# Performance work log

Measured on AMD Instinct MI355X. Metric: run time of the kernel, lower is better.

The kernel has to match this reference:

```python
import jax, jax.numpy as jnp
import numpy as np

B, IN, U = 16, 1024, 1024


def _wSw(W, S):
    # W: [i,u], S: [b,i,i] -> W^T S W : [b,u,u]
    return jnp.einsum('iu,bij,jv->buv', W, S, W)


def _xSx(x, Wsig):
    # (sum_i x_i^2) * W_Sigma, broadcast over batch
    return jnp.sum(x * x, axis=1)[:, None, None] * Wsig


def _trS(S, Wsig):
    return jnp.trace(S, axis1=1, axis2=2)[:, None, None] * Wsig


def _hadamard_sigma(s1, s2, m1, m2):
    # s1*s2 + diag(m1) s2 diag(m1) + diag(m2) s1 diag(m2)
    return (s1 * s2
            + m1[:, :, None] * s2 * m1[:, None, :]
            + m2[:, :, None] * s1 * m2[:, None, :])


def _act_sigma(g, S):
    # S * outer(g, g)
    return S * (g[:, :, None] * g[:, None, :])


def setup_inputs() -> dict:
    key = jax.random.key(0)
    ks = jax.random.split(key, 16)
    f32 = jnp.float32
    init_mu, ini_sigma = 0.05, -4.6
    inp = {
        'mu_inputs': jax.random.normal(ks[0], (B, IN), f32),
        'sigma_inputs': 0.01 * jax.random.normal(ks[1], (B, IN, IN), f32),
        'prev_state': 0.1 * jax.random.normal(ks[2], (B, U), f32),
        'Sigma_state': 0.01 * jax.random.normal(ks[3], (B, U, U), f32),
        'U_z': init_mu * jax.random.normal(ks[4], (IN, U), f32),
        'uz_sigma': jnp.full((U,), ini_sigma, f32),
        'W_z': init_mu * jax.random.normal(ks[5], (U, U), f32),
        'wz_sigma': jnp.full((U,), ini_sigma, f32),
        'U_r': init_mu * jax.random.normal(ks[6], (IN, U), f32),
        'ur_sigma': jnp.full((U,), ini_sigma, f32),
        'W_r': init_mu * jax.random.normal(ks[7], (U, U), f32),
        'wr_sigma': jnp.full((U,), ini_sigma, f32),
        'U_h': init_mu * jax.random.normal(ks[8], (IN, U), f32),
        'uh_sigma': jnp.full((U,), ini_sigma, f32),
        'W_h': init_mu * jax.random.normal(ks[9], (U, U), f32),
        'wh_sigma': jnp.full((U,), ini_sigma, f32),
    }
    return inp


def reference(mu_inputs, sigma_inputs, prev_state, Sigma_state,
              U_z, uz_sigma, W_z, wz_sigma,
              U_r, ur_sigma, W_r, wr_sigma,
              U_h, uh_sigma, W_h, wh_sigma):
    sp = jax.nn.softplus
    # ---- z gate ----
    pre_z = mu_inputs @ U_z + prev_state @ W_z
    z = jax.nn.sigmoid(pre_z)
    Uz_S, Wz_S = jnp.diag(sp(uz_sigma)), jnp.diag(sp(wz_sigma))
    Sigma_zz = (_wSw(U_z, sigma_inputs) + _xSx(mu_inputs, Uz_S) + _trS(sigma_inputs, Uz_S)
                + _wSw(W_z, Sigma_state) + _xSx(prev_state, Wz_S) + _trS(Sigma_state, Wz_S))
    Sigma_z = _act_sigma(z * (1.0 - z), Sigma_zz)  # analytic d sigmoid
    # ---- r gate ----
    pre_r = mu_inputs @ U_r + prev_state @ W_r
    r = jax.nn.sigmoid(pre_r)
    Ur_S, Wr_S = jnp.diag(sp(ur_sigma)), jnp.diag(sp(wr_sigma))
    Sigma_rr = (_wSw(U_r, sigma_inputs) + _xSx(mu_inputs, Ur_S) + _trS(sigma_inputs, Ur_S)
                + _wSw(W_r, Sigma_state) + _xSx(prev_state, Wr_S) + _trS(Sigma_state, Wr_S))
    Sigma_r = _act_sigma(r * (1.0 - r), Sigma_rr)
    # ---- h gate ----
    sr = prev_state * r
    pre_h = mu_inputs @ U_h + sr @ W_h
    h = jnp.tanh(pre_h)
    Uh_S, Wh_S = jnp.diag(sp(uh_sigma)), jnp.diag(sp(wh_sigma))
    sigma_g = _hadamard_sigma(Sigma_state, Sigma_r, prev_state, r)
    Sigma_hh = (_wSw(U_h, sigma_inputs) + _xSx(mu_inputs, Uh_S) + _trS(sigma_inputs, Uh_S)
                + _wSw(W_h, sigma_g) + _xSx(sr, Wh_S) + _trS(sigma_g, Wh_S))
    Sigma_h = _act_sigma(1.0 - h * h, Sigma_hh)  # analytic d tanh
    # ---- combine ----
    mu_out = z * prev_state + (1.0 - z) * h
    sigma_a = _hadamard_sigma(Sigma_z, Sigma_state, z, prev_state)
    sigma_b = _hadamard_sigma(Sigma_z, Sigma_h, 1.0 - z, h)
    sigma_ab = Sigma_z * (prev_state[:, :, None] * h[:, None, :])
    sigma_abT = Sigma_z * (h[:, :, None] * prev_state[:, None, :])
    Sigma_out = sigma_a + sigma_b - sigma_ab - sigma_abT
    Sigma_out = jnp.where(jnp.isfinite(Sigma_out), Sigma_out, jnp.zeros_like(Sigma_out))
    eye = jnp.eye(Sigma_out.shape[-1], dtype=bool)
    Sigma_out = jnp.where(eye, jnp.abs(Sigma_out), Sigma_out)
    return mu_out, Sigma_out
```

## Files before the change

kernel.cpp:

```cpp
#include <hip/hip_runtime.h>
#include <math.h>


#define B_  16
#define N_  1024
#define NN_ (1024*1024)

typedef __bf16 bf16x8 __attribute__((ext_vector_type(8)));
typedef float  f32x4  __attribute__((ext_vector_type(4)));
typedef unsigned short ushort8v __attribute__((ext_vector_type(8)));

__device__ __forceinline__ unsigned short f2bf(float f) {
  union { float f; unsigned int u; } v; v.f = f;
  unsigned int r = v.u + 0x7fffu + ((v.u >> 16) & 1u);
  return (unsigned short)(r >> 16);
}
__device__ __forceinline__ float bf2f(unsigned short h) {
  union { unsigned int u; float f; } v; v.u = ((unsigned int)h) << 16;
  return v.f;
}

__device__ __forceinline__ void gload_lds16(const void* g, void* l) {
  __builtin_amdgcn_global_load_lds((__attribute__((address_space(1))) void*)g,
                                   (__attribute__((address_space(3))) void*)l,
                                   16, 0, 0);
}

#define MFMA_ __builtin_amdgcn_mfma_f32_16x16x32_bf16
#define SYNC_()  do { asm volatile("s_waitcnt lgkmcnt(0)" ::: "memory"); \
                      __builtin_amdgcn_sched_barrier(0); \
                      __builtin_amdgcn_s_barrier(); \
                      __builtin_amdgcn_sched_barrier(0); } while (0)

template<int OMODE, int PAIR>
__global__ __launch_bounds__(512)
void gemm8p(const unsigned short* __restrict__ A, int lda, long aStride, int koffA,
            const unsigned short* __restrict__ Bm, const unsigned short* __restrict__ Bm2,
            int ldb, long bStride, int K,
            void* __restrict__ Out, int ldo, long oStride, int noff,
            const float* __restrict__ act,
            const float* __restrict__ spU, const float* __restrict__ spW,
            const float* __restrict__ dU, const float* __restrict__ dW,
            const unsigned short* __restrict__ SzP, const float* __restrict__ SstP,
            const float* __restrict__ zV, const float* __restrict__ prevV,
            const float* __restrict__ hV)
{
  __shared__ __align__(16) char ldsb[131072];
  const int id = blockIdx.x;
  const int xcd = id & 7, rest = id >> 3;
  const int mt = rest & 3, pp = rest >> 2;
  const int panel = xcd + (pp << 3);
  const int nt = panel & 3;
  const int b  = (panel >> 2) & 15;
  const int ps = PAIR ? (panel >> 6) : 0;
  const unsigned short* Bsel = (PAIR && ps) ? Bm2 : Bm;
  const int kofx = koffA + (ps ? 1024 : 0);
  const int nofx = noff  + (ps ? 1024 : 0);
  const int mbase = mt << 8, nbase = nt << 8;
  const int tid = threadIdx.x, lane = tid & 63, w = tid >> 6;
  const int wm = w >> 2, wn = w & 3;
  const int NT = K >> 6;

  f32x4 acc[8][4];
  const f32x4 zero4 = {0.f, 0.f, 0.f, 0.f};
#pragma unroll
  for (int i = 0; i < 8; i++)
#pragma unroll
    for (int j = 0; j < 4; j++) acc[i][j] = zero4;

  const int l3 = lane >> 3, l7 = lane & 7;
  const int posg = l7 ^ l3;
  const int gr = (l3 << 1) + (posg >> 2);
  const int gc = (posg & 3) << 3;
  const int bi0 = w << 1, bi1 = bi0 + 1;
  const int rS0 = ((bi0 >> 1) << 4) + gr, cS0 = ((bi0 & 1) << 5) + gc;
  const int rS1 = ((bi1 >> 1) << 4) + gr, cS1 = ((bi1 & 1) << 5) + gc;
  const unsigned short* Ab = A + (size_t)b * aStride + (size_t)mbase * lda + kofx;
  const unsigned short* Bb = Bsel + (size_t)b * bStride + (size_t)nbase * ldb;
  const int d0 = w << 11, d1 = (w << 11) + 1024;

  auto SA = [&](int tt, int h) {
    char* dst = ldsb + ((tt & 1) << 16) + (h << 14);
    const unsigned short* s = Ab + (size_t)(h << 7) * lda + ((size_t)tt << 6);
    gload_lds16(s + (size_t)rS0 * lda + cS0, dst + d0);
    gload_lds16(s + (size_t)rS1 * lda + cS1, dst + d1);
  };
  auto SB = [&](int tt, int h) {
    char* dst = ldsb + ((tt & 1) << 16) + 32768 + (h << 14);
    const unsigned short* s = Bb + (size_t)(h << 7) * ldb + ((size_t)tt << 6);
    gload_lds16(s + (size_t)rS0 * ldb + cS0, dst + d0);
    gload_lds16(s + (size_t)rS1 * ldb + cS1, dst + d1);
  };

  const int lrow = lane & 15, c4 = lane >> 4;
  const int aoff = ((lrow >> 1) << 7) + (((((lrow & 1) << 2) | c4) ^ (lrow >> 1)) << 4);
  const int abase = wm << 14;
  const int bbase = 32768 + ((wn >> 1) << 14);
  const int brg   = (wn & 1) << 2;
  auto LDA = [&](const char* pb, int mi, int ks) -> bf16x8 {
    return *(const bf16x8*)(pb + abase + (((mi << 1) + ks) << 10) + aoff);
  };
  auto LDB = [&](const char* pb, int ni, int ks) -> bf16x8 {
    return *(const bf16x8*)(pb + bbase + ((((brg + ni) << 1) + ks) << 10) + aoff);
  };

  SA(0, 0); SA(0, 1); SB(0, 0); SB(0, 1);
  if (NT > 1) { SB(1, 0); SB(1, 1); }
  asm volatile("s_waitcnt vmcnt(4)" ::: "memory");
  __builtin_amdgcn_sched_barrier(0);
  __builtin_amdgcn_s_barrier();
  __builtin_amdgcn_sched_barrier(0);

  bf16x8 avA[4], avB[4], bvA[4], bvB[4];
#pragma unroll
  for (int i = 0; i < 4; i++) avB[i] = LDA(ldsb, i, 0);
#pragma unroll
  for (int i = 0; i < 4; i++) bvB[i] = LDB(ldsb, i, 0);
  __builtin_amdgcn_sched_barrier(0);

  for (int kt = 0; kt < NT; ++kt) {
    const char* pb = ldsb + ((kt & 1) << 16);
    const char* pn = ldsb + (((kt + 1) & 1) << 16);
#pragma unroll
    for (int i = 0; i < 4; i++) avA[i] = LDA(pb, 4 + i, 0);
    if (kt + 1 < NT) SA(kt + 1, 0);
    __builtin_amdgcn_s_setprio(1);
#pragma unroll
    for (int ni = 0; ni < 4; ni++)
#pragma unroll
      for (int mi = 0; mi < 4; mi++)
        acc[mi][ni] = MFMA_(avB[mi], bvB[ni], acc[mi][ni], 0, 0, 0);
    __builtin_amdgcn_s_setprio(0);
#pragma unroll
    for (int i = 0; i < 4; i++) avB[i] = LDA(pb, i, 1);
#pragma unroll
    for (int i = 0; i < 4; i++) bvA[i] = LDB(pb, i, 1);
    if (kt + 1 < NT) SA(kt + 1, 1);
    __builtin_amdgcn_s_setprio(1);
#pragma unroll
    for (int ni = 0; ni < 4; ni++)
#pragma unroll
      for (int mi = 0; mi < 4; mi++)
        acc[4 + mi][ni] = MFMA_(avA[mi], bvB[ni], acc[4 + mi][ni], 0, 0, 0);
    __builtin_amdgcn_s_setprio(0);
    SYNC_();
#pragma unroll
    for (int i = 0; i < 4; i++) avA[i] = LDA(pb, 4 + i, 1);
    __builtin_amdgcn_s_setprio(1);
#pragma unroll
    for (int ni = 0; ni < 4; ni++)
#pragma unroll
      for (int mi = 0; mi < 4; mi++)
        acc[mi][ni] = MFMA_(avB[mi], bvA[ni], acc[mi][ni], 0, 0, 0);
    __builtin_amdgcn_s_setprio(0);
    if (kt + 2 < NT) {
      SB(kt + 2, 0); SB(kt + 2, 1);
      asm volatile("s_waitcnt vmcnt(4)" ::: "memory");
    } else {
      asm volatile("s_waitcnt vmcnt(0)" ::: "memory");
    }
    SYNC_();
    if (kt + 1 < NT) {
#pragma unroll
      for (int i = 0; i < 4; i++) avB[i] = LDA(pn, i, 0);
#pragma unroll
      for (int i = 0; i < 4; i++) bvB[i] = LDB(pn, i, 0);
    }
    __builtin_amdgcn_sched_barrier(0);
    __builtin_amdgcn_s_setprio(1);
#pragma unroll
    for (int ni = 0; ni < 4; ni++)
#pragma unroll
      for (int mi = 0; mi < 4; mi++)
        acc[4 + mi][ni] = MFMA_(avA[mi], bvA[ni], acc[4 + mi][ni], 0, 0, 0);
    __builtin_amdgcn_s_setprio(0);
  }

  __syncthreads();
  unsigned short* scr = (unsigned short*)(ldsb + w * 16384);
  const float* actb = act ? (act + b * N_) : nullptr;
  float dUb = 0.f, dWb = 0.f;
  if (OMODE != 0) { dUb = dU[b]; dWb = dW[b]; }

#pragma unroll
  for (int mi = 0; mi < 8; mi++) {
    const int rl0 = mi * 16 + ((lane >> 4) << 2);
#pragma unroll
    for (int ni = 0; ni < 4; ni++) {
      const int cl = ni * 16 + (lane & 15);
#pragma unroll
      for (int r = 0; r < 4; r++) {
        const int rl = rl0 + r;
        float val = acc[mi][ni][r];
        if (OMODE != 0) {
          const int u = mbase + wm * 128 + rl, v = nbase + wn * 64 + cl;
          if (u == v) val += dUb * spU[u] + dWb * spW[u];
          val *= actb[u] * actb[v];
        }
        scr[rl * 64 + ((((cl >> 3) ^ (rl & 7))) << 3) + (cl & 7)] = f2bf(val);
      }
    }
  }
  asm volatile("s_waitcnt lgkmcnt(0)" ::: "memory");
  __builtin_amdgcn_sched_barrier(0);

#pragma unroll
  for (int pq = 0; pq < 16; pq++) {
    const int row = pq * 8 + (lane >> 3);
    const int slot = lane & 7;
    const int ch = slot ^ (row & 7);
    const int u = mbase + wm * 128 + row;
    const int v0 = nbase + wn * 64 + (ch << 3);
    ushort8v s8 = *(const ushort8v*)&scr[row * 64 + (slot << 3)];
    if (OMODE == 0 || OMODE == 1) {
      unsigned short* ob = (unsigned short*)Out + (size_t)b * oStride
                         + (size_t)u * ldo + nofx + v0;
      *(ushort8v*)ob = s8;
    } else if (OMODE == 3) {
      const float pu = prevV[b * N_ + u];
      const float ru = zV[b * N_ + u];
      const ushort8v st8 = *(const ushort8v*)(SzP + (size_t)b * NN_ + (size_t)u * N_ + v0);
      const f32x4 pv0 = *(const f32x4*)(prevV + b * N_ + v0);
      const f32x4 pv1 = *(const f32x4*)(prevV + b * N_ + v0 + 4);
      const f32x4 rv0 = *(const f32x4*)(zV + b * N_ + v0);
      const f32x4 rv1 = *(const f32x4*)(zV + b * N_ + v0 + 4);
      ushort8v o8;
#pragma unroll
      for (int q = 0; q < 8; q++) {
        const float srv = bf2f((unsigned short)s8[q]);
        const float stt = bf2f((unsigned short)st8[q]);
        const float pv = (q < 4) ? pv0[q] : pv1[q - 4];
        const float rv = (q < 4) ? rv0[q] : rv1[q - 4];
        o8[q] = f2bf(stt * srv + pu * pv * srv + ru * rv * stt);
      }
      unsigned short* ob = (unsigned short*)Out + (size_t)b * oStride
                         + (size_t)u * ldo + v0;
      *(ushort8v*)ob = o8;
    } else {
      const float zu = zV[b * N_ + u];
      const float pu = prevV[b * N_ + u];
      const float hu = hV[b * N_ + u];
      const ushort8v sz8 = *(const ushort8v*)(SzP + (size_t)b * NN_ + (size_t)u * N_ + v0);
      const f32x4 st0 = *(const f32x4*)(SstP + (size_t)b * NN_ + (size_t)u * N_ + v0);
      const f32x4 st1 = *(const f32x4*)(SstP + (size_t)b * NN_ + (size_t)u * N_ + v0 + 4);
      const f32x4 zv0 = *(const f32x4*)(zV + b * N_ + v0);
      const f32x4 zv1 = *(const f32x4*)(zV + b * N_ + v0 + 4);
      const f32x4 pv0 = *(const f32x4*)(prevV + b * N_ + v0);
      const f32x4 pv1 = *(const f32x4*)(prevV + b * N_ + v0 + 4);
      const f32x4 hv0 = *(const f32x4*)(hV + b * N_ + v0);
      const f32x4 hv1 = *(const f32x4*)(hV + b * N_ + v0 + 4);
      f32x4 o0, o1;
#pragma unroll
      for (int q = 0; q < 8; q++) {
        const float shh = bf2f((unsigned short)s8[q]);
        const float szv = bf2f((unsigned short)sz8[q]);
        const float stt = (q < 4) ? st0[q] : st1[q - 4];
        const float zv  = (q < 4) ? zv0[q] : zv1[q - 4];
        const float pv  = (q < 4) ? pv0[q] : pv1[q - 4];
        const float hv  = (q < 4) ? hv0[q] : hv1[q - 4];
        float res = szv * stt + zu * zv * stt + pu * pv * szv
                  + szv * shh + (1.f - zu) * (1.f - zv) * shh + hu * hv * szv
                  - szv * (pu * hv) - szv * (hu * pv);
        if (!isfinite(res)) res = 0.f;
        if (u == v0 + q) res = fabsf(res);
        if (q < 4) o0[q] = res; else o1[q - 4] = res;
      }
      float* ob = (float*)Out + (size_t)b * oStride + (size_t)u * ldo + v0;
      *(f32x4*)ob = o0;
      *(f32x4*)(ob + 4) = o1;
    }
  }
}


__global__ void conv_bf16_2(const float* __restrict__ in0, unsigned short* __restrict__ out0,
                            const float* __restrict__ in1, unsigned short* __restrict__ out1,
                            int n4)
{
  const float* in = blockIdx.y ? in1 : in0;
  unsigned short* out = blockIdx.y ? out1 : out0;
  int i = blockIdx.x * 256 + threadIdx.x;
  const int stride = gridDim.x * 256;
  for (; i < n4; i += stride) {
    const float4 v = ((const float4*)in)[i];
    ushort4 o;
    o.x = f2bf(v.x); o.y = f2bf(v.y); o.z = f2bf(v.z); o.w = f2bf(v.w);
    ((ushort4*)out)[i] = o;
  }
}

__global__ void build_AT(const float* __restrict__ Uz, const float* __restrict__ Wz,
                         const float* __restrict__ Ur, const float* __restrict__ Wr,
                         const float* __restrict__ Uh, const float* __restrict__ Wh,
                         unsigned short* __restrict__ AT)
{
  __shared__ float tile[32][33];
  const int g = blockIdx.z;
  const float* U = g == 0 ? Uz : (g == 1 ? Ur : Uh);
  const float* W = g == 0 ? Wz : (g == 1 ? Wr : Wh);
  const int u0  = blockIdx.x * 32;
  const int k0g = blockIdx.y * 32;
  const float* src = (k0g >= 1024) ? W : U;
  const int kloc = k0g & 1023;
  const int tx = threadIdx.x & 31, ty = threadIdx.x >> 5;
  unsigned short* out = AT + (size_t)g * N_ * 2048;
#pragma unroll
  for (int i = 0; i < 32; i += 8) tile[ty + i][tx] = src[(size_t)(kloc + ty + i) * N_ + u0 + tx];
  __syncthreads();
#pragma unroll
  for (int i = 0; i < 32; i += 8)
    out[(size_t)(u0 + ty + i) * 2048 + k0g + tx] = f2bf(tile[tx][ty + i]);
}

__global__ void softplus6(const float* a0, const float* a1, const float* a2,
                          const float* a3, const float* a4, const float* a5,
                          float* __restrict__ sp)
{
  const float* src[6] = {a0, a1, a2, a3, a4, a5};
  const int g = blockIdx.x;
  const float* s = src[g];
  for (int i = threadIdx.x; i < N_; i += 256) {
    float x = s[i];
    sp[g * N_ + i] = (x > 20.f) ? x : log1pf(expf(x));
  }
}

__global__ void scalars1(const float* __restrict__ mu, const float* __restrict__ prev,
                         const float* __restrict__ sin_, const float* __restrict__ Sst,
                         float* __restrict__ dA, float* __restrict__ dBzr)
{
  __shared__ float red[256];
  const int b = blockIdx.x;
  float s1 = 0.f, s2 = 0.f;
  for (int i = threadIdx.x; i < N_; i += 256) {
    const float m = mu[b * N_ + i];
    s1 += m * m + sin_[(size_t)b * NN_ + (size_t)i * (N_ + 1)];
    const float p = prev[b * N_ + i];
    s2 += p * p + Sst[(size_t)b * NN_ + (size_t)i * (N_ + 1)];
  }
  red[threadIdx.x] = s1; __syncthreads();
  for (int s = 128; s > 0; s >>= 1) { if (threadIdx.x < s) red[threadIdx.x] += red[threadIdx.x + s]; __syncthreads(); }
  if (threadIdx.x == 0) dA[b] = red[0];
  __syncthreads();
  red[threadIdx.x] = s2; __syncthreads();
  for (int s = 128; s > 0; s >>= 1) { if (threadIdx.x < s) red[threadIdx.x] += red[threadIdx.x + s]; __syncthreads(); }
  if (threadIdx.x == 0) dBzr[b] = red[0];
}

__global__ __launch_bounds__(256)
void gate_pre2(const float* __restrict__ x1, const float* __restrict__ x2,
               const float* __restrict__ U0, const float* __restrict__ W0,
               const float* __restrict__ U1, const float* __restrict__ W1,
               float* __restrict__ Ppart)
{
  const int g  = blockIdx.z;
  const int ks = blockIdx.y;
  const int out = blockIdx.x * 256 + threadIdx.x;
  const int b = out >> 10, col = out & 1023;
  const float* x = (ks < 4) ? x1 : x2;
  const float* Wm = (g == 0) ? ((ks < 4) ? U0 : W0) : ((ks < 4) ? U1 : W1);
  const int k0 = (ks & 3) * 256;
  const float* xb = x + b * N_ + k0;
  const float* wp = Wm + (size_t)k0 * N_ + col;
  float acc = 0.f;
#pragma unroll 8
  for (int k = 0; k < 256; k++)
    acc += xb[k] * wp[(size_t)k * N_];
  Ppart[(g * 8 + ks) * (B_ * N_) + out] = acc;
}

__global__ void gate_act2(const float* __restrict__ P,
                          float* __restrict__ z, float* __restrict__ gz,
                          float* __restrict__ r, float* __restrict__ gr)
{
  const int out = blockIdx.x * 256 + threadIdx.x;
  float a0 = 0.f, a1 = 0.f;
#pragma unroll
  for (int ks = 0; ks < 8; ks++) {
    a0 += P[ks * (B_ * N_) + out];
    a1 += P[(8 + ks) * (B_ * N_) + out];
  }
  const float s0 = 1.f / (1.f + expf(-a0));
  const float s1 = 1.f / (1.f + expf(-a1));
  z[out] = s0; gz[out] = s0 * (1.f - s0);
  r[out] = s1; gr[out] = s1 * (1.f - s1);
}

__global__ __launch_bounds__(256)
void gate_pre1(const float* __restrict__ x1, const float* __restrict__ x2,
               const float* __restrict__ U0, const float* __restrict__ W0,
               float* __restrict__ Ppart)
{
  const int ks = blockIdx.y;
  const int out = blockIdx.x * 256 + threadIdx.x;
  const int b = out >> 10, col = out & 1023;
  const float* x = (ks < 4) ? x1 : x2;
  const float* Wm = (ks < 4) ? U0 : W0;
  const int k0 = (ks & 3) * 256;
  const float* xb = x + b * N_ + k0;
  const float* wp = Wm + (size_t)k0 * N_ + col;
  float acc = 0.f;
#pragma unroll 8
  for (int k = 0; k < 256; k++)
    acc += xb[k] * wp[(size_t)k * N_];
  Ppart[ks * (B_ * N_) + out] = acc;
}

__global__ void gate_act1(const float* __restrict__ P,
                          const float* __restrict__ z, const float* __restrict__ prev,
                          float* __restrict__ h, float* __restrict__ gh,
                          float* __restrict__ mu_out)
{
  const int out = blockIdx.x * 256 + threadIdx.x;
  float a0 = 0.f;
#pragma unroll
  for (int ks = 0; ks < 8; ks++) a0 += P[ks * (B_ * N_) + out];
  const float s = tanhf(a0);
  h[out] = s; gh[out] = 1.f - s * s;
  const float zz = z[out];
  mu_out[out] = zz * prev[out] + (1.f - zz) * s;
}

__global__ void sr_csr(const float* __restrict__ prev, const float* __restrict__ r,
                       float* __restrict__ sr, float* __restrict__ csr)
{
  __shared__ float red[256];
  const int b = blockIdx.x;
  float s = 0.f;
  for (int i = threadIdx.x; i < N_; i += 256) {
    const float v = prev[b * N_ + i] * r[b * N_ + i];
    sr[b * N_ + i] = v;
    s += v * v;
  }
  red[threadIdx.x] = s; __syncthreads();
  for (int k = 128; k > 0; k >>= 1) { if (threadIdx.x < k) red[threadIdx.x] += red[threadIdx.x + k]; __syncthreads(); }
  if (threadIdx.x == 0) csr[b] = red[0];
}

__global__ void scalars2(const unsigned short* __restrict__ Sg,
                         const float* __restrict__ csr, float* __restrict__ dBh)
{
  __shared__ float red[256];
  const int b = blockIdx.x;
  float s = 0.f;
  for (int i = threadIdx.x; i < N_; i += 256)
    s += bf2f(Sg[(size_t)b * NN_ + (size_t)i * (N_ + 1)]);
  red[threadIdx.x] = s; __syncthreads();
  for (int k = 128; k > 0; k >>= 1) { if (threadIdx.x < k) red[threadIdx.x] += red[threadIdx.x + k]; __syncthreads(); }
  if (threadIdx.x == 0) dBh[b] = red[0] + csr[b];
}


extern "C" void kernel_launch(void* const* d_in, const int* in_sizes, int n_in,
                              void* d_out, int out_size, void* d_ws, size_t ws_size,
                              hipStream_t stream)
{
  const float* mu   = (const float*)d_in[0];
  const float* sin_ = (const float*)d_in[1];
  const float* prev = (const float*)d_in[2];
  const float* Sst  = (const float*)d_in[3];
  const float* Uz = (const float*)d_in[4];  const float* uzs = (const float*)d_in[5];
  const float* Wz = (const float*)d_in[6];  const float* wzs = (const float*)d_in[7];
  const float* Ur = (const float*)d_in[8];  const float* urs = (const float*)d_in[9];
  const float* Wr = (const float*)d_in[10]; const float* wrs = (const float*)d_in[11];
  const float* Uh = (const float*)d_in[12]; const float* uhs = (const float*)d_in[13];
  const float* Wh = (const float*)d_in[14]; const float* whs = (const float*)d_in[15];

  char* ws = (char*)d_ws;
  size_t off = 0;
  auto take = [&](size_t bytes) -> char* {
    char* p = ws + off;
    off = (off + bytes + 255) & ~(size_t)255;
    return p;
  };
  unsigned short* Tcm = (unsigned short*)take((size_t)B_ * 2048 * 1024 * 2);
  unsigned short* Sz  = (unsigned short*)take((size_t)B_ * NN_ * 2);
  unsigned short* Sg  = (unsigned short*)take((size_t)B_ * NN_ * 2);
  unsigned short* AT  = (unsigned short*)take((size_t)3 * N_ * 2048 * 2);
  float* Ppart = (float*)take((size_t)16 * B_ * N_ * 4);
  float* sp   = (float*)take(6 * N_ * 4);
  float* z    = (float*)take(B_ * N_ * 4);
  float* gz   = (float*)take(B_ * N_ * 4);
  float* rr   = (float*)take(B_ * N_ * 4);
  float* gr   = (float*)take(B_ * N_ * 4);
  float* h    = (float*)take(B_ * N_ * 4);
  float* gh   = (float*)take(B_ * N_ * 4);
  float* sr   = (float*)take(B_ * N_ * 4);
  float* dA   = (float*)take(64);
  float* dBzr = (float*)take(64);
  float* dBh  = (float*)take(64);
  float* csr  = (float*)take(64);
  if (off > ws_size) return;

  float* mu_out = (float*)d_out;
  float* SigOut = (float*)d_out + (size_t)B_ * N_;
  unsigned short* SinH = (unsigned short*)SigOut;
  unsigned short* SstH = (unsigned short*)SigOut + (size_t)B_ * NN_;

  const unsigned short* ATz = AT;
  const unsigned short* ATr = AT + (size_t)N_ * 2048;
  const unsigned short* ATh = AT + (size_t)2 * N_ * 2048;

  conv_bf16_2<<<dim3(2048, 2), 256, 0, stream>>>(sin_, SinH, Sst, SstH, B_ * NN_ / 4);
  softplus6<<<6, 256, 0, stream>>>(uzs, wzs, urs, wrs, uhs, whs, sp);
  scalars1<<<16, 256, 0, stream>>>(mu, prev, sin_, Sst, dA, dBzr);
  build_AT<<<dim3(32, 64, 3), 256, 0, stream>>>(Uz, Wz, Ur, Wr, Uh, Wh, AT);
  gate_pre2<<<dim3(64, 8, 2), 256, 0, stream>>>(mu, prev, Uz, Wz, Ur, Wr, Ppart);
  gate_act2<<<64, 256, 0, stream>>>(Ppart, z, gz, rr, gr);
  sr_csr<<<16, 256, 0, stream>>>(prev, rr, sr, csr);
  gate_pre1<<<dim3(64, 8), 256, 0, stream>>>(mu, sr, Uh, Wh, Ppart);
  gate_act1<<<64, 256, 0, stream>>>(Ppart, z, prev, h, gh, mu_out);

  const long tS = (long)2048 * 1024;

  gemm8p<0, 1><<<512, 512, 0, stream>>>(ATz, 2048, 0, 0, SinH, SstH, 1024, (long)NN_, 1024,
                                        Tcm, 2048, tS, 0, nullptr, nullptr, nullptr, nullptr, nullptr,
                                        nullptr, nullptr, nullptr, nullptr, nullptr);
  gemm8p<1, 0><<<256, 512, 0, stream>>>(ATz, 2048, 0, 0, Tcm, nullptr, 2048, tS, 2048,
                                        Sz, 1024, (long)NN_, 0, gz, sp + 0, sp + 1024, dA, dBzr,
                                        nullptr, nullptr, nullptr, nullptr, nullptr);
  gemm8p<0, 1><<<512, 512, 0, stream>>>(ATr, 2048, 0, 0, SinH, SstH, 1024, (long)NN_, 1024,
                                        Tcm, 2048, tS, 0, nullptr, nullptr, nullptr, nullptr, nullptr,
                                        nullptr, nullptr, nullptr, nullptr, nullptr);
  gemm8p<3, 0><<<256, 512, 0, stream>>>(ATr, 2048, 0, 0, Tcm, nullptr, 2048, tS, 2048,
                                        Sg, 1024, (long)NN_, 0, gr, sp + 2048, sp + 3072, dA, dBzr,
                                        SstH, nullptr, rr, prev, nullptr);
  scalars2<<<16, 256, 0, stream>>>(Sg, csr, dBh);
  gemm8p<0, 1><<<512, 512, 0, stream>>>(ATh, 2048, 0, 0, SinH, Sg, 1024, (long)NN_, 1024,
                                        Tcm, 2048, tS, 0, nullptr, nullptr, nullptr, nullptr, nullptr,
                                        nullptr, nullptr, nullptr, nullptr, nullptr);
  gemm8p<2, 0><<<256, 512, 0, stream>>>(ATh, 2048, 0, 0, Tcm, nullptr, 2048, tS, 2048,
                                        SigOut, 1024, (long)NN_, 0, gh, sp + 4096, sp + 5120, dA, dBh,
                                        Sz, Sst, z, prev, h);
}
```

Before: 513.4 us.

## Triple-buffer B tiles in LDS to drop a mid-iteration barrier

Shrinks each A stage to 32KB, double-buffering A while triple-buffering the B operand in LDS, which grows shared memory to 160KB. Because B for step kt+2 now lands in a slot separate from the one being read, the workgroup barrier between the second and third MFMA phases is removed. The aim is less barrier stall per K-step in the batched GEMM. The cost is using the full LDS budget per CU, which rules out co-resident blocks and adds modulo-3 slot bookkeeping.

```diff
diff --git a/kernel.cpp b/kernel.cpp
--- a/kernel.cpp
+++ b/kernel.cpp
@@ -45,7 +45,7 @@
             const float* __restrict__ zV, const float* __restrict__ prevV,
             const float* __restrict__ hV)
 {
-  __shared__ __align__(16) char ldsb[131072];
+  __shared__ __align__(16) char ldsb[163840];
   const int id = blockIdx.x;
   const int xcd = id & 7, rest = id >> 3;
   const int mt = rest & 3, pp = rest >> 2;
@@ -80,13 +80,13 @@
   const int d0 = w << 11, d1 = (w << 11) + 1024;
 
   auto SA = [&](int tt, int h) {
-    char* dst = ldsb + ((tt & 1) << 16) + (h << 14);
+    char* dst = ldsb + ((tt & 1) << 15) + (h << 14);
     const unsigned short* s = Ab + (size_t)(h << 7) * lda + ((size_t)tt << 6);
     gload_lds16(s + (size_t)rS0 * lda + cS0, dst + d0);
     gload_lds16(s + (size_t)rS1 * lda + cS1, dst + d1);
   };
   auto SB = [&](int tt, int h) {
-    char* dst = ldsb + ((tt & 1) << 16) + 32768 + (h << 14);
+    char* dst = ldsb + 65536 + (tt % 3) * 32768 + (h << 14);
     const unsigned short* s = Bb + (size_t)(h << 7) * ldb + ((size_t)tt << 6);
     gload_lds16(s + (size_t)rS0 * ldb + cS0, dst + d0);
     gload_lds16(s + (size_t)rS1 * ldb + cS1, dst + d1);
@@ -95,13 +95,13 @@
   const int lrow = lane & 15, c4 = lane >> 4;
   const int aoff = ((lrow >> 1) << 7) + (((((lrow & 1) << 2) | c4) ^ (lrow >> 1)) << 4);
   const int abase = wm << 14;
-  const int bbase = 32768 + ((wn >> 1) << 14);
+  const int bbase = ((wn >> 1) << 14);
   const int brg   = (wn & 1) << 2;
-  auto LDA = [&](const char* pb, int mi, int ks) -> bf16x8 {
-    return *(const bf16x8*)(pb + abase + (((mi << 1) + ks) << 10) + aoff);
+  auto LDA = [&](const char* pa, int mi, int ks) -> bf16x8 {
+    return *(const bf16x8*)(pa + abase + (((mi << 1) + ks) << 10) + aoff);
   };
-  auto LDB = [&](const char* pb, int ni, int ks) -> bf16x8 {
-    return *(const bf16x8*)(pb + bbase + ((((brg + ni) << 1) + ks) << 10) + aoff);
+  auto LDB = [&](const char* pbv, int ni, int ks) -> bf16x8 {
+    return *(const bf16x8*)(pbv + bbase + ((((brg + ni) << 1) + ks) << 10) + aoff);
   };
 
   SA(0, 0); SA(0, 1); SB(0, 0); SB(0, 1);
@@ -115,14 +115,18 @@
 #pragma unroll
   for (int i = 0; i < 4; i++) avB[i] = LDA(ldsb, i, 0);
 #pragma unroll
-  for (int i = 0; i < 4; i++) bvB[i] = LDB(ldsb, i, 0);
+  for (int i = 0; i < 4; i++) bvB[i] = LDB(ldsb + 65536, i, 0);
   __builtin_amdgcn_sched_barrier(0);
 
+  int bs = 0;
   for (int kt = 0; kt < NT; ++kt) {
-    const char* pb = ldsb + ((kt & 1) << 16);
-    const char* pn = ldsb + (((kt + 1) & 1) << 16);
-#pragma unroll
-    for (int i = 0; i < 4; i++) avA[i] = LDA(pb, 4 + i, 0);
+    const char* pa = ldsb + ((kt & 1) << 15);
+    const char* pbv = ldsb + 65536 + bs * 32768;
+    const int bsn = (bs == 2) ? 0 : bs + 1;
+    const char* pan = ldsb + (((kt + 1) & 1) << 15);
+    const char* pbn = ldsb + 65536 + bsn * 32768;
+#pragma unroll
+    for (int i = 0; i < 4; i++) avA[i] = LDA(pa, 4 + i, 0);
     if (kt + 1 < NT) SA(kt + 1, 0);
     __builtin_amdgcn_s_setprio(1);
 #pragma unroll
@@ -132,9 +136,9 @@
         acc[mi][ni] = MFMA_(avB[mi], bvB[ni], acc[mi][ni], 0, 0, 0);
     __builtin_amdgcn_s_setprio(0);
 #pragma unroll
-    for (int i = 0; i < 4; i++) avB[i] = LDA(pb, i, 1);
-#pragma unroll
-    for (int i = 0; i < 4; i++) bvA[i] = LDB(pb, i, 1);
+    for (int i = 0; i < 4; i++) avB[i] = LDA(pa, i, 1);
+#pragma unroll
+    for (int i = 0; i < 4; i++) bvA[i] = LDB(pbv, i, 1);
     if (kt + 1 < NT) SA(kt + 1, 1);
     __builtin_amdgcn_s_setprio(1);
 #pragma unroll
@@ -143,9 +147,8 @@
       for (int mi = 0; mi < 4; mi++)
         acc[4 + mi][ni] = MFMA_(avA[mi], bvB[ni], acc[4 + mi][ni], 0, 0, 0);
     __builtin_amdgcn_s_setprio(0);
-    SYNC_();
-#pragma unroll
-    for (int i = 0; i < 4; i++) avA[i] = LDA(pb, 4 + i, 1);
+#pragma unroll
+    for (int i = 0; i < 4; i++) avA[i] = LDA(pa, 4 + i, 1);
     __builtin_amdgcn_s_setprio(1);
 #pragma unroll
     for (int ni = 0; ni < 4; ni++)
@@ -162,9 +165,9 @@
     SYNC_();
     if (kt + 1 < NT) {
 #pragma unroll
-      for (int i = 0; i < 4; i++) avB[i] = LDA(pn, i, 0);
-#pragma unroll
-      for (int i = 0; i < 4; i++) bvB[i] = LDB(pn, i, 0);
+      for (int i = 0; i < 4; i++) avB[i] = LDA(pan, i, 0);
+#pragma unroll
+      for (int i = 0; i < 4; i++) bvB[i] = LDB(pbn, i, 0);
     }
     __builtin_amdgcn_sched_barrier(0);
     __builtin_amdgcn_s_setprio(1);
@@ -174,6 +177,7 @@
       for (int mi = 0; mi < 4; mi++)
         acc[4 + mi][ni] = MFMA_(avA[mi], bvA[ni], acc[4 + mi][ni], 0, 0, 0);
     __builtin_amdgcn_s_setprio(0);
+    bs = bsn;
   }
 
   __syncthreads();
```

New measurement: 514.6 us (median of 2 runs). No clear change (+0.2%).
